# Kernel tuning notes

Hardware: AMD Instinct MI355X
Metric: run time of the kernel (lower is better)

Reference implementation:

```python
import jax, jax.numpy as jnp
import numpy as np

N, S, D = 8, 1024, 512      # batch, seq_len, in_dim
H, KD, VD, OD = 8, 64, 64, 512  # heads, key_dim, value_dim, out_dim
GRAPH_WEIGHT = 0.5
NEG_INF = float('-inf')


def setup_inputs() -> dict:
    key = jax.random.key(0)
    ks = jax.random.split(key, 9)
    return {
        "x":    jax.random.normal(ks[0], (N, S, D), jnp.float32),
        "Wk":   jax.random.normal(ks[1], (H, D, KD), jnp.float32) * 0.02,
        "bk":   jax.random.normal(ks[2], (H, KD), jnp.float32) * 0.02,
        "Wv":   jax.random.normal(ks[3], (H, D, VD), jnp.float32) * 0.02,
        "bv":   jax.random.normal(ks[4], (H, VD), jnp.float32) * 0.02,
        "Wout": jax.random.normal(ks[5], (H * VD, OD), jnp.float32) * 0.02,
        "bout": jax.random.normal(ks[6], (OD,), jnp.float32) * 0.02,
        "graph": jax.random.normal(ks[7], (S, S), jnp.float32),
        "knn": 64,
    }


def reference(x, Wk, bk, Wv, bv, Wout, bout, graph, knn):
    # Per-head key/value projections (heads vectorized on leading axis h).
    k = jnp.einsum('nsd,hdk->hnsk', x, Wk) + bk[:, None, None, :]   # (H,N,S,KD)
    v = jnp.einsum('nsd,hdv->hnsv', x, Wv) + bv[:, None, None, :]   # (H,N,S,VD)
    q = k  # self-attention: query = key

    # att_unnorm = (q . k) / sqrt(key_dim)  -> (H,N,S,S)
    att = jnp.einsum('hnqk,hntk->hnqt', q, k) / np.sqrt(KD).astype(np.float32)

    # Causal mask (equivalent to the Python loop att[:, i, i+1:] = -inf).
    causal = jnp.tril(jnp.ones((S, S), dtype=bool))
    att = jnp.where(causal, att, NEG_INF)

    # knn top-k pooling: keep top-knn entries along the last axis, rest -> -inf.
    topv = jax.lax.top_k(att, knn)[0]                  # (H,N,S,knn)
    kth = topv[..., -1:]                               # kth largest per row
    att = jnp.where(att >= kth, att, NEG_INF)

    p = jax.nn.softmax(att, axis=-1)

    # Graph-weighted attention blend (graph is row-softmaxed at init time).
    att_graph = jax.nn.softmax(graph, axis=-1)         # (S,S)
    p = GRAPH_WEIGHT * att_graph + (1.0 - GRAPH_WEIGHT) * p

    # y_h = att @ value, then concat heads and output projection.
    y = jnp.einsum('hnqt,hntv->hnqv', p, v)            # (H,N,S,VD)
    y = y.transpose(1, 2, 0, 3).reshape(N, S, H * VD)  # head-major concat
    return y @ Wout + bout
```

## Files before the change

kernel.cpp:

```cpp
#include <hip/hip_runtime.h>
#include <math.h>

#define NB 8
#define SL 1024
#define DI 512
#define HH 8
#define KDN 64
#define VDN 64
#define ODN 512
#define ATT_SCALE 0.125f

#define KLO_OFF 2097152u
#define V_OFF   4194304u
#define G_OFF   8388608u
#define Y_OFF   9437184u

#define ORD_NEG_INF 0x007FFFFFu

typedef __attribute__((ext_vector_type(8))) short bf16x8;
typedef __attribute__((ext_vector_type(4))) float f32x4;

__device__ __forceinline__ unsigned fordu(float f) {
  unsigned b = __float_as_uint(f);
  return b ^ ((b & 0x80000000u) ? 0xFFFFFFFFu : 0x80000000u);
}
__device__ __forceinline__ float ifordu(unsigned k) {
  unsigned b = k ^ ((k & 0x80000000u) ? 0x80000000u : 0xFFFFFFFFu);
  return __uint_as_float(b);
}
__device__ __forceinline__ unsigned short f2bf(float f) {
  unsigned u = __float_as_uint(f);
  unsigned r = (u + 0x7FFFu + ((u >> 16) & 1u)) >> 16;
  return (unsigned short)r;
}
__device__ __forceinline__ float bf2f(unsigned short h) {
  return __uint_as_float(((unsigned)h) << 16);
}

__global__ __launch_bounds__(256) void kvproj_kernel(
    const float* __restrict__ x, const float* __restrict__ Wk, const float* __restrict__ bk,
    const float* __restrict__ Wv, const float* __restrict__ bv, float* __restrict__ ws)
{
  __shared__ float xs[64][68];
  __shared__ float wks[64][68];
  __shared__ float wvs[64][68];
  const int tid = threadIdx.x;
  const int tx = tid & 15, ty = tid >> 4;
  const int m0 = blockIdx.x * 64;
  const int h = blockIdx.y;
  const float* wkb = Wk + (size_t)h * (DI * KDN);
  const float* wvb = Wv + (size_t)h * (DI * VDN);
  float ak[4][4] = {{0.f}};
  float av[4][4] = {{0.f}};
  for (int dt = 0; dt < DI / 64; ++dt) {
    __syncthreads();
#pragma unroll
    for (int it = 0; it < 4; ++it) {
      const int r = ty + it * 16;
      const int c = tx * 4;
      *(float4*)&xs[r][c]  = *(const float4*)&x[(size_t)(m0 + r) * DI + dt * 64 + c];
      *(float4*)&wks[r][c] = *(const float4*)&wkb[(size_t)(dt * 64 + r) * KDN + c];
      *(float4*)&wvs[r][c] = *(const float4*)&wvb[(size_t)(dt * 64 + r) * VDN + c];
    }
    __syncthreads();
#pragma unroll 4
    for (int dd = 0; dd < 64; ++dd) {
      float a[4];
#pragma unroll
      for (int i = 0; i < 4; ++i) a[i] = xs[ty * 4 + i][dd];
      const float4 bkv = *(const float4*)&wks[dd][tx * 4];
      const float4 bvv = *(const float4*)&wvs[dd][tx * 4];
      const float bkj[4] = {bkv.x, bkv.y, bkv.z, bkv.w};
      const float bvj[4] = {bvv.x, bvv.y, bvv.z, bvv.w};
#pragma unroll
      for (int i = 0; i < 4; ++i) {
#pragma unroll
        for (int j = 0; j < 4; ++j) {
          ak[i][j] = __fmaf_rn(a[i], bkj[j], ak[i][j]);
          av[i][j] = __fmaf_rn(a[i], bvj[j], av[i][j]);
        }
      }
    }
  }
  const int n = m0 >> 10;
  const int s0 = m0 & 1023;
  float* vb = ws + V_OFF;
  unsigned short* khi = (unsigned short*)ws;
  unsigned short* klo = (unsigned short*)(ws + KLO_OFF);
#pragma unroll
  for (int i = 0; i < 4; ++i) {
    const int s = s0 + ty * 4 + i;
    float4 vv;
    vv.x = av[i][0] + bv[h * VDN + tx * 4 + 0];
    vv.y = av[i][1] + bv[h * VDN + tx * 4 + 1];
    vv.z = av[i][2] + bv[h * VDN + tx * 4 + 2];
    vv.w = av[i][3] + bv[h * VDN + tx * 4 + 3];
    *(float4*)&vb[((size_t)(h * NB + n) * SL + s) * VDN + tx * 4] = vv;
    union { unsigned short u[4]; uint2 v2; } ph, pl;
#pragma unroll
    for (int j = 0; j < 4; ++j) {
      const float kf = ak[i][j] + bk[h * KDN + tx * 4 + j];
      const unsigned short h16 = f2bf(kf);
      ph.u[j] = h16;
      pl.u[j] = f2bf(kf - bf2f(h16));
    }
    const size_t koff = ((size_t)(h * NB + n) * SL + s) * KDN + tx * 4;
    *(uint2*)&khi[koff] = ph.v2;
    *(uint2*)&klo[koff] = pl.v2;
  }
}

__global__ __launch_bounds__(256) void gsoftmax_kernel(const float* __restrict__ gin, float* __restrict__ ws)
{
  float* gout = ws + G_OFF;
  const int row = blockIdx.x;
  const int tid = threadIdx.x;
  const int lane = tid & 63, wave = tid >> 6;
  __shared__ float red[4];
  __shared__ float red2[4];
  float v[4];
  float m = -INFINITY;
#pragma unroll
  for (int i = 0; i < 4; ++i) {
    v[i] = gin[(size_t)row * SL + tid + i * 256];
    m = fmaxf(m, v[i]);
  }
#pragma unroll
  for (int off = 32; off; off >>= 1) m = fmaxf(m, __shfl_xor(m, off));
  if (lane == 0) red[wave] = m;
  __syncthreads();
  m = fmaxf(fmaxf(red[0], red[1]), fmaxf(red[2], red[3]));
  float e[4];
  float s = 0.f;
#pragma unroll
  for (int i = 0; i < 4; ++i) { e[i] = __expf(v[i] - m); s += e[i]; }
#pragma unroll
  for (int off = 32; off; off >>= 1) s += __shfl_xor(s, off);
  if (lane == 0) red2[wave] = s;
  __syncthreads();
  s = red2[0] + red2[1] + red2[2] + red2[3];
  const float inv = 1.0f / s;
#pragma unroll
  for (int i = 0; i < 4; ++i) gout[(size_t)row * SL + tid + i * 256] = e[i] * inv;
}

__global__ __launch_bounds__(512, 4) void attn_kernel(float* __restrict__ ws, const int* __restrict__ knn_p)
{
  __shared__ float S[16][260];
  const int tid = threadIdx.x;
  const int lane = tid & 63;
  const int wave = tid >> 6;
  const int q0 = blockIdx.x * 16;
  const int hn = blockIdx.y;
  const int h = hn >> 3, n = hn & 7;
  const int K = knn_p[0];
  const unsigned short* khi = (const unsigned short*)ws + (size_t)hn * SL * KDN;
  const unsigned short* klo = (const unsigned short*)(ws + KLO_OFF) + (size_t)hn * SL * KDN;
  const float* vb = ws + V_OFF + (size_t)hn * (SL * VDN);
  float* y = ws + Y_OFF;

  const int col = lane & 15, grp = lane >> 4;
  const bf16x8 a0h = *(const bf16x8*)&khi[(size_t)(q0 + col) * KDN + grp * 8];
  const bf16x8 a1h = *(const bf16x8*)&khi[(size_t)(q0 + col) * KDN + 32 + grp * 8];
  const bf16x8 a0l = *(const bf16x8*)&klo[(size_t)(q0 + col) * KDN + grp * 8];
  const bf16x8 a1l = *(const bf16x8*)&klo[(size_t)(q0 + col) * KDN + 32 + grp * 8];

  const int T = q0 / 16 + 1;
  const int rbase = wave * 2;

  float ev[2][8][2];
#pragma unroll
  for (int rr = 0; rr < 2; ++rr)
#pragma unroll
    for (int c = 0; c < 8; ++c) {
      ev[rr][c][0] = __uint_as_float(ORD_NEG_INF);
      ev[rr][c][1] = __uint_as_float(ORD_NEG_INF);
    }

#pragma unroll
  for (int ph = 0; ph < 4; ++ph) {
    const int tlo = ph * 16;
    const int thi = (T < tlo + 16) ? T : (tlo + 16);
    if (thi > tlo) {
      __syncthreads();
      for (int ti = tlo + wave; ti < thi; ti += 8) {
        const int t0 = ti * 16;
        const size_t bo = (size_t)(t0 + col) * KDN + grp * 8;
        const bf16x8 b0h = *(const bf16x8*)&khi[bo];
        const bf16x8 b1h = *(const bf16x8*)&khi[bo + 32];
        const bf16x8 b0l = *(const bf16x8*)&klo[bo];
        const bf16x8 b1l = *(const bf16x8*)&klo[bo + 32];
        f32x4 d = {0.f, 0.f, 0.f, 0.f};
        d = __builtin_amdgcn_mfma_f32_16x16x32_bf16(a0h, b0h, d, 0, 0, 0);
        d = __builtin_amdgcn_mfma_f32_16x16x32_bf16(a1h, b1h, d, 0, 0, 0);
        d = __builtin_amdgcn_mfma_f32_16x16x32_bf16(a0h, b0l, d, 0, 0, 0);
        d = __builtin_amdgcn_mfma_f32_16x16x32_bf16(a1h, b1l, d, 0, 0, 0);
        d = __builtin_amdgcn_mfma_f32_16x16x32_bf16(a0l, b0h, d, 0, 0, 0);
        d = __builtin_amdgcn_mfma_f32_16x16x32_bf16(a1l, b1h, d, 0, 0, 0);
        d = __builtin_amdgcn_mfma_f32_16x16x32_bf16(a0l, b0l, d, 0, 0, 0);
        d = __builtin_amdgcn_mfma_f32_16x16x32_bf16(a1l, b1l, d, 0, 0, 0);
        const int tl = t0 - ph * 256 + col;
#pragma unroll
        for (int r = 0; r < 4; ++r) S[grp * 4 + r][tl] = d[r];
      }
      __syncthreads();
#pragma unroll
      for (int rr = 0; rr < 2; ++rr) {
        const int q = q0 + rbase + rr;
        const int cmr = q >> 7;
#pragma unroll
        for (int cc = 0; cc < 2; ++cc) {
          const int c = ph * 2 + cc;
          if (c <= cmr) {
            const float2 sv = *(const float2*)&S[rbase + rr][cc * 128 + lane * 2];
            const int t0 = c * 128 + lane * 2;
            const unsigned k0 = (t0     <= q) ? fordu(sv.x * ATT_SCALE) : ORD_NEG_INF;
            const unsigned k1 = (t0 + 1 <= q) ? fordu(sv.y * ATT_SCALE) : ORD_NEG_INF;
            ev[rr][c][0] = __uint_as_float(k0);
            ev[rr][c][1] = __uint_as_float(k1);
          }
        }
      }
    }
  }
  __syncthreads();

  float* elist = (float*)((char*)&S[0][0] + wave * 768);
  unsigned short* tlist = (unsigned short*)(elist + 128);

#pragma unroll
  for (int rr = 0; rr < 2; ++rr) {
    const int q = q0 + rbase + rr;

    unsigned u[16];
#pragma unroll
    for (int c = 0; c < 8; ++c) {
      u[c * 2]     = __float_as_uint(ev[rr][c][0]);
      u[c * 2 + 1] = __float_as_uint(ev[rr][c][1]);
    }

    unsigned lmax = u[0];
#pragma unroll
    for (int i = 1; i < 16; ++i) lmax = lmax > u[i] ? lmax : u[i];
    unsigned mk = lmax, t0k = lmax;
#pragma unroll
    for (int off = 32; off; off >>= 1) {
      const unsigned om = (unsigned)__shfl_xor((int)mk, off);
      const unsigned ot = (unsigned)__shfl_xor((int)t0k, off);
      mk = mk > om ? mk : om;
      t0k = t0k < ot ? t0k : ot;
    }
    const float m = ifordu(mk);

    unsigned kth;
    if (q < K) {
      kth = ORD_NEG_INF;
    } else {
      unsigned lo = (K <= 64) ? t0k : 0u;
      unsigned hi = mk;
      while (lo < hi) {
        const unsigned mid = lo + ((hi - lo + 1) >> 1);
        int cnt = 0;
#pragma unroll
        for (int i = 0; i < 16; ++i)
          cnt += (int)__popcll(__ballot(u[i] >= mid));
        if (cnt >= K) lo = mid; else hi = mid - 1;
      }
      kth = lo;
    }

    float Z = 0.f;
#pragma unroll
    for (int c = 0; c < 8; ++c) {
#pragma unroll
      for (int j = 0; j < 2; ++j) {
        const unsigned k = u[c * 2 + j];
        float e = 0.f;
        if (k >= kth) e = __expf(ifordu(k) - m);
        ev[rr][c][j] = e;
        Z += e;
      }
    }
#pragma unroll
    for (int off = 32; off; off >>= 1) Z += __shfl_xor(Z, off);

    const unsigned long long lt = (1ull << lane) - 1ull;
    int cnt = 0;
#pragma unroll
    for (int c = 0; c < 8; ++c) {
#pragma unroll
      for (int j = 0; j < 2; ++j) {
        const float e = ev[rr][c][j];
        const unsigned long long msk = __ballot(e > 0.f);
        if (e > 0.f) {
          const int pos = cnt + (int)__popcll(msk & lt);
          if (pos < 128) {
            elist[pos] = e;
            tlist[pos] = (unsigned short)(c * 128 + lane * 2 + j);
          }
        }
        cnt += (int)__popcll(msk);
      }
    }
    cnt = (cnt < 128) ? cnt : 128;

    float yacc = 0.f;
    int i2 = 0;
    for (; i2 + 4 <= cnt; i2 += 4) {
      const float4 e4 = *(const float4*)&elist[i2];
      const ushort4 t4 = *(const ushort4*)&tlist[i2];
      yacc = __fmaf_rn(e4.x, vb[(size_t)t4.x * VDN + lane], yacc);
      yacc = __fmaf_rn(e4.y, vb[(size_t)t4.y * VDN + lane], yacc);
      yacc = __fmaf_rn(e4.z, vb[(size_t)t4.z * VDN + lane], yacc);
      yacc = __fmaf_rn(e4.w, vb[(size_t)t4.w * VDN + lane], yacc);
    }
    for (; i2 < cnt; ++i2) {
      yacc = __fmaf_rn(elist[i2], vb[(size_t)tlist[i2] * VDN + lane], yacc);
    }
    y[((size_t)(n * SL + q)) * ODN + h * VDN + lane] = yacc * (0.5f / Z);
  }
}

__global__ __launch_bounds__(256) void gv_kernel(float* __restrict__ ws)
{
  __shared__ float as_[64][68];
  __shared__ float bs_[64][68];
  const int tid = threadIdx.x;
  const int tx = tid & 15, ty = tid >> 4;
  const int q0 = blockIdx.x * 64;
  const int hn = blockIdx.y;
  const int h = hn >> 3, n = hn & 7;
  const float* g = ws + G_OFF;
  const float* vb = ws + V_OFF + (size_t)hn * (SL * VDN);
  float* y = ws + Y_OFF;
  float acc[4][4] = {{0.f}};
  for (int kt = 0; kt < 16; ++kt) {
    __syncthreads();
#pragma unroll
    for (int it = 0; it < 4; ++it) {
      const int r = ty + it * 16;
      const int c = tx * 4;
      *(float4*)&as_[r][c] = *(const float4*)&g[(size_t)(q0 + r) * SL + kt * 64 + c];
      *(float4*)&bs_[r][c] = *(const float4*)&vb[(size_t)(kt * 64 + r) * VDN + c];
    }
    __syncthreads();
#pragma unroll 4
    for (int dd = 0; dd < 64; ++dd) {
      float a[4];
#pragma unroll
      for (int i = 0; i < 4; ++i) a[i] = as_[ty * 4 + i][dd];
      const float4 b4 = *(const float4*)&bs_[dd][tx * 4];
      const float bj[4] = {b4.x, b4.y, b4.z, b4.w};
#pragma unroll
      for (int i = 0; i < 4; ++i)
#pragma unroll
        for (int j = 0; j < 4; ++j)
          acc[i][j] = __fmaf_rn(a[i], bj[j], acc[i][j]);
    }
  }
#pragma unroll
  for (int i = 0; i < 4; ++i) {
    const size_t off = ((size_t)(n * SL + q0 + ty * 4 + i)) * ODN + h * VDN + tx * 4;
    float4 cur = *(float4*)&y[off];
    cur.x += 0.5f * acc[i][0];
    cur.y += 0.5f * acc[i][1];
    cur.z += 0.5f * acc[i][2];
    cur.w += 0.5f * acc[i][3];
    *(float4*)&y[off] = cur;
  }
}

__global__ __launch_bounds__(256) void wtprep_kernel(const float* __restrict__ Wout, float* __restrict__ ws)
{
  __shared__ float tile[64][65];
  unsigned short* wth = (unsigned short*)ws;
  unsigned short* wtl = wth + ODN * ODN;
  const int t = threadIdx.x;
  const int od0 = blockIdx.x * 64;
  const int k0 = blockIdx.y * 64;
  const int r = t >> 2, c4 = (t & 3) * 16;
#pragma unroll
  for (int j = 0; j < 4; ++j) {
    *(float4*)&tile[r][c4 + j * 4] = *(const float4*)&Wout[(size_t)(k0 + r) * ODN + od0 + c4 + j * 4];
  }
  __syncthreads();
  union { unsigned short u[16]; uint4 v[2]; } hi, lo;
#pragma unroll
  for (int j = 0; j < 16; ++j) {
    const float f = tile[c4 + j][r];
    const unsigned short h16 = f2bf(f);
    hi.u[j] = h16;
    lo.u[j] = f2bf(f - bf2f(h16));
  }
  const size_t o = (size_t)(od0 + r) * ODN + k0 + c4;
  *(uint4*)&wth[o] = hi.v[0];
  *(uint4*)&wth[o + 8] = hi.v[1];
  *(uint4*)&wtl[o] = lo.v[0];
  *(uint4*)&wtl[o + 8] = lo.v[1];
}

__global__ __launch_bounds__(256) void out_kernel(
    const float* __restrict__ bout, const float* __restrict__ ws, float* __restrict__ out)
{
  const unsigned short* wth = (const unsigned short*)ws;
  const unsigned short* wtl = wth + ODN * ODN;
  const float* y = ws + Y_OFF;
  const int tid = threadIdx.x;
  const int lane = tid & 63;
  const int wave = tid >> 6;
  const int col = lane & 15, grp = lane >> 4;
  const int od0 = blockIdx.x * 64;
  const int m0 = blockIdx.y * 64 + wave * 16;

  f32x4 acc[4];
#pragma unroll
  for (int odt = 0; odt < 4; ++odt) acc[odt] = (f32x4){0.f, 0.f, 0.f, 0.f};

  const float* yrow = y + (size_t)(m0 + col) * ODN + grp * 8;
  for (int ks = 0; ks < 16; ++ks) {
    const float4 ya = *(const float4*)&yrow[ks * 32];
    const float4 yb = *(const float4*)&yrow[ks * 32 + 4];
    union { unsigned short u[8]; bf16x8 v; } ah, al;
    const float yf[8] = {ya.x, ya.y, ya.z, ya.w, yb.x, yb.y, yb.z, yb.w};
#pragma unroll
    for (int j = 0; j < 8; ++j) {
      const unsigned short h16 = f2bf(yf[j]);
      ah.u[j] = h16;
      al.u[j] = f2bf(yf[j] - bf2f(h16));
    }
#pragma unroll
    for (int odt = 0; odt < 4; ++odt) {
      const size_t bo = (size_t)(od0 + odt * 16 + col) * ODN + ks * 32 + grp * 8;
      const bf16x8 bh = *(const bf16x8*)&wth[bo];
      const bf16x8 bl = *(const bf16x8*)&wtl[bo];
      acc[odt] = __builtin_amdgcn_mfma_f32_16x16x32_bf16(ah.v, bh, acc[odt], 0, 0, 0);
      acc[odt] = __builtin_amdgcn_mfma_f32_16x16x32_bf16(ah.v, bl, acc[odt], 0, 0, 0);
      acc[odt] = __builtin_amdgcn_mfma_f32_16x16x32_bf16(al.v, bh, acc[odt], 0, 0, 0);
    }
  }

#pragma unroll
  for (int odt = 0; odt < 4; ++odt) {
    const int od = od0 + odt * 16 + col;
    const float bo = bout[od];
#pragma unroll
    for (int r = 0; r < 4; ++r) {
      out[(size_t)(m0 + grp * 4 + r) * ODN + od] = acc[odt][r] + bo;
    }
  }
}

extern "C" void kernel_launch(void* const* d_in, const int* in_sizes, int n_in,
                              void* d_out, int out_size, void* d_ws, size_t ws_size,
                              hipStream_t stream)
{
  const float* x     = (const float*)d_in[0];
  const float* Wk    = (const float*)d_in[1];
  const float* bk    = (const float*)d_in[2];
  const float* Wv    = (const float*)d_in[3];
  const float* bv    = (const float*)d_in[4];
  const float* Wout  = (const float*)d_in[5];
  const float* bout  = (const float*)d_in[6];
  const float* graph = (const float*)d_in[7];
  const int*   knn   = (const int*)d_in[8];
  float* out = (float*)d_out;
  float* ws  = (float*)d_ws;

  kvproj_kernel<<<dim3(128, 8), 256, 0, stream>>>(x, Wk, bk, Wv, bv, ws);
  gsoftmax_kernel<<<dim3(1024), 256, 0, stream>>>(graph, ws);
  attn_kernel<<<dim3(64, 64), 512, 0, stream>>>(ws, knn);
  wtprep_kernel<<<dim3(8, 8), 256, 0, stream>>>(Wout, ws);
  gv_kernel<<<dim3(16, 64), 256, 0, stream>>>(ws);
  out_kernel<<<dim3(8, 128), 256, 0, stream>>>(bout, ws, out);
}
```

Measured before the change: 553.3 us.

## Compute graph-weighted value product with bf16 MFMA instead of fp32 FMA

Result: faster. 511.0 us (-7.6%).

```diff
diff --git a/kernel.cpp b/kernel.cpp
--- a/kernel.cpp
+++ b/kernel.cpp
@@ -112,7 +112,7 @@
 
 __global__ __launch_bounds__(256) void gsoftmax_kernel(const float* __restrict__ gin, float* __restrict__ ws)
 {
-  float* gout = ws + G_OFF;
+  unsigned short* ghi = (unsigned short*)(ws + G_OFF);
   const int row = blockIdx.x;
   const int tid = threadIdx.x;
   const int lane = tid & 63, wave = tid >> 6;
@@ -141,7 +141,7 @@
   s = red2[0] + red2[1] + red2[2] + red2[3];
   const float inv = 1.0f / s;
 #pragma unroll
-  for (int i = 0; i < 4; ++i) gout[(size_t)row * SL + tid + i * 256] = e[i] * inv;
+  for (int i = 0; i < 4; ++i) ghi[(size_t)row * SL + tid + i * 256] = f2bf(e[i] * inv);
 }
 
 __global__ __launch_bounds__(512, 4) void attn_kernel(float* __restrict__ ws, const int* __restrict__ knn_p)
@@ -321,59 +321,69 @@
   }
 }
 
+__global__ __launch_bounds__(256) void vtprep_kernel(float* __restrict__ ws)
+{
+  __shared__ float tile[64][65];
+  const int t = threadIdx.x;
+  const int t0 = blockIdx.x * 64;
+  const int hn = blockIdx.y;
+  const float* vb = ws + V_OFF + (size_t)hn * (SL * VDN);
+  unsigned short* vthi = (unsigned short*)ws + (size_t)hn * VDN * SL;
+  const int r = t >> 2, c4 = (t & 3) * 16;
+#pragma unroll
+  for (int j = 0; j < 4; ++j)
+    *(float4*)&tile[r][c4 + j * 4] = *(const float4*)&vb[(size_t)(t0 + r) * VDN + c4 + j * 4];
+  __syncthreads();
+  union { unsigned short u[16]; uint4 v[2]; } hi;
+#pragma unroll
+  for (int j = 0; j < 16; ++j) hi.u[j] = f2bf(tile[c4 + j][r]);
+  const size_t o = (size_t)r * SL + t0 + c4;
+  *(uint4*)&vthi[o] = hi.v[0];
+  *(uint4*)&vthi[o + 8] = hi.v[1];
+}
+
 __global__ __launch_bounds__(256) void gv_kernel(float* __restrict__ ws)
 {
-  __shared__ float as_[64][68];
-  __shared__ float bs_[64][68];
+  const unsigned short* ghi = (const unsigned short*)(ws + G_OFF);
   const int tid = threadIdx.x;
-  const int tx = tid & 15, ty = tid >> 4;
+  const int lane = tid & 63;
+  const int wave = tid >> 6;
+  const int col = lane & 15, grp = lane >> 4;
   const int q0 = blockIdx.x * 64;
   const int hn = blockIdx.y;
   const int h = hn >> 3, n = hn & 7;
-  const float* g = ws + G_OFF;
-  const float* vb = ws + V_OFF + (size_t)hn * (SL * VDN);
+  const unsigned short* vthi = (const unsigned short*)ws + (size_t)hn * VDN * SL;
   float* y = ws + Y_OFF;
-  float acc[4][4] = {{0.f}};
-  for (int kt = 0; kt < 16; ++kt) {
-    __syncthreads();
-#pragma unroll
-    for (int it = 0; it < 4; ++it) {
-      const int r = ty + it * 16;
-      const int c = tx * 4;
-      *(float4*)&as_[r][c] = *(const float4*)&g[(size_t)(q0 + r) * SL + kt * 64 + c];
-      *(float4*)&bs_[r][c] = *(const float4*)&vb[(size_t)(kt * 64 + r) * VDN + c];
-    }
-    __syncthreads();
-#pragma unroll 4
-    for (int dd = 0; dd < 64; ++dd) {
-      float a[4];
-#pragma unroll
-      for (int i = 0; i < 4; ++i) a[i] = as_[ty * 4 + i][dd];
-      const float4 b4 = *(const float4*)&bs_[dd][tx * 4];
-      const float bj[4] = {b4.x, b4.y, b4.z, b4.w};
-#pragma unroll
-      for (int i = 0; i < 4; ++i)
-#pragma unroll
-        for (int j = 0; j < 4; ++j)
-          acc[i][j] = __fmaf_rn(a[i], bj[j], acc[i][j]);
-    }
-  }
-#pragma unroll
-  for (int i = 0; i < 4; ++i) {
-    const size_t off = ((size_t)(n * SL + q0 + ty * 4 + i)) * ODN + h * VDN + tx * 4;
-    float4 cur = *(float4*)&y[off];
-    cur.x += 0.5f * acc[i][0];
-    cur.y += 0.5f * acc[i][1];
-    cur.z += 0.5f * acc[i][2];
-    cur.w += 0.5f * acc[i][3];
-    *(float4*)&y[off] = cur;
+
+  f32x4 acc[4];
+#pragma unroll
+  for (int odt = 0; odt < 4; ++odt) acc[odt] = (f32x4){0.f, 0.f, 0.f, 0.f};
+
+  const size_t arow = (size_t)(q0 + wave * 16 + col) * SL;
+  for (int ks = 0; ks < 32; ++ks) {
+    const bf16x8 ah = *(const bf16x8*)&ghi[arow + ks * 32 + grp * 8];
+#pragma unroll
+    for (int odt = 0; odt < 4; ++odt) {
+      const bf16x8 bh = *(const bf16x8*)&vthi[(size_t)(odt * 16 + col) * SL + ks * 32 + grp * 8];
+      acc[odt] = __builtin_amdgcn_mfma_f32_16x16x32_bf16(ah, bh, acc[odt], 0, 0, 0);
+    }
+  }
+
+#pragma unroll
+  for (int odt = 0; odt < 4; ++odt) {
+    const int vd = odt * 16 + col;
+#pragma unroll
+    for (int r = 0; r < 4; ++r) {
+      const size_t off = ((size_t)(n * SL + q0 + wave * 16 + grp * 4 + r)) * ODN + h * VDN + vd;
+      y[off] += 0.5f * acc[odt][r];
+    }
   }
 }
 
 __global__ __launch_bounds__(256) void wtprep_kernel(const float* __restrict__ Wout, float* __restrict__ ws)
 {
   __shared__ float tile[64][65];
-  unsigned short* wth = (unsigned short*)ws;
+  unsigned short* wth = (unsigned short*)(ws + KLO_OFF);
   unsigned short* wtl = wth + ODN * ODN;
   const int t = threadIdx.x;
   const int od0 = blockIdx.x * 64;
@@ -402,7 +412,7 @@
 __global__ __launch_bounds__(256) void out_kernel(
     const float* __restrict__ bout, const float* __restrict__ ws, float* __restrict__ out)
 {
-  const unsigned short* wth = (const unsigned short*)ws;
+  const unsigned short* wth = (const unsigned short*)(ws + KLO_OFF);
   const unsigned short* wtl = wth + ODN * ODN;
   const float* y = ws + Y_OFF;
   const int tid = threadIdx.x;
@@ -469,6 +479,7 @@
   kvproj_kernel<<<dim3(128, 8), 256, 0, stream>>>(x, Wk, bk, Wv, bv, ws);
   gsoftmax_kernel<<<dim3(1024), 256, 0, stream>>>(graph, ws);
   attn_kernel<<<dim3(64, 64), 512, 0, stream>>>(ws, knn);
+  vtprep_kernel<<<dim3(16, 64), 256, 0, stream>>>(ws);
   wtprep_kernel<<<dim3(8, 8), 256, 0, stream>>>(Wout, ws);
   gv_kernel<<<dim3(16, 64), 256, 0, stream>>>(ws);
   out_kernel<<<dim3(8, 128), 256, 0, stream>>>(bout, ws, out);
```
